# Kernel tuning notes

Measured on AMD Instinct MI355X. Metric: run time of the kernel, lower is better.

Reference implementation:

```python
import jax, jax.numpy as jnp
import numpy as np

EPS = 1e-8  # matches torch cosine_similarity default eps


def setup_inputs() -> dict:
    key = jax.random.key(0)
    k1, k2 = jax.random.split(key)
    B, S, D = 64, 512, 768
    logits = jax.random.normal(k1, (B, S, D), dtype=jnp.float32)
    labels = jax.random.randint(k2, (B, S), 0, 10, dtype=jnp.int64)
    return {"logits": logits, "labels": labels, "entity_id": 5}


def reference(logits, labels, entity_id):
    # --- get_proto: mean of token vectors whose label == entity_id,
    # excluding sequence position 0 (label_idx.remove(0) in the original) ---
    B, S, D = logits.shape
    pos = jnp.arange(S)
    ent_mask = (labels == entity_id) & (pos[None, :] != 0)      # [B,S]
    m = ent_mask.astype(logits.dtype)
    num_ent = jnp.maximum(m.sum(), 1.0)
    proto = jnp.einsum('bs,bsd->d', m, logits) / num_ent        # [D]

    # --- CLLoss: mean cosine similarity between proto and every token
    # with a nonzero label ---
    nz_mask = (labels != 0).astype(logits.dtype)                # [B,S]
    dots = jnp.einsum('bsd,d->bs', logits, proto)               # [B,S]
    denom = jnp.linalg.norm(logits, axis=-1) * jnp.linalg.norm(proto)
    sims = dots / jnp.maximum(denom, EPS)                       # [B,S]
    num_tok = jnp.maximum(nz_mask.sum(), 1.0)
    loss = (sims * nz_mask).sum() / num_tok
    return loss
```

## Files before the change

kernel.cpp:

```cpp
#include <hip/hip_runtime.h>
#include <math.h>

#define DD 768
#define S_LEN 512
#define NF4 3

__global__ __launch_bounds__(256) void zero_acc(float* acc, int n) {
    int i = blockIdx.x * 256 + threadIdx.x;
    if (i < n) acc[i] = 0.f;
}

__global__ __launch_bounds__(256) void main_pass(const float* __restrict__ logits,
                                                 const int* __restrict__ labels,
                                                 const int* __restrict__ eid_p,
                                                 int ntok,
                                                 float* __restrict__ acc) {
    const int eid  = *eid_p;
    const int lane = threadIdx.x & 63;
    const int wid  = threadIdx.x >> 6;
    const int gw   = blockIdx.x * 4 + wid;
    const int nw   = gridDim.x * 4;

    float u_acc[12], p_acc[12];
#pragma unroll
    for (int j = 0; j < 12; ++j) { u_acc[j] = 0.f; p_acc[j] = 0.f; }
    float tokcnt = 0.f;

    for (int t = gw; t < ntok; t += nw) {
        const float4* src = (const float4*)(logits + (size_t)t * DD);
        float4 f[NF4];
#pragma unroll
        for (int k = 0; k < NF4; ++k) f[k] = src[k * 64 + lane];

        float ss = 0.f;
#pragma unroll
        for (int k = 0; k < NF4; ++k)
            ss += f[k].x * f[k].x + f[k].y * f[k].y + f[k].z * f[k].z + f[k].w * f[k].w;
#pragma unroll
        for (int o = 32; o > 0; o >>= 1) ss += __shfl_xor(ss, o, 64);

        const int lbl = labels[t];
        const float inv = (ss > 0.f) ? rsqrtf(ss) : 0.f;
        const float wu  = (lbl != 0) ? inv : 0.f;
        const float wp  = (lbl == eid && (t & (S_LEN - 1)) != 0) ? 1.f : 0.f;
        tokcnt += (lbl != 0) ? 1.f : 0.f;

#pragma unroll
        for (int k = 0; k < NF4; ++k) {
            u_acc[4 * k + 0] += f[k].x * wu;  p_acc[4 * k + 0] += f[k].x * wp;
            u_acc[4 * k + 1] += f[k].y * wu;  p_acc[4 * k + 1] += f[k].y * wp;
            u_acc[4 * k + 2] += f[k].z * wu;  p_acc[4 * k + 2] += f[k].z * wp;
            u_acc[4 * k + 3] += f[k].w * wu;  p_acc[4 * k + 3] += f[k].w * wp;
        }
    }

    __shared__ float sh[2 * DD + 1];
    for (int i = threadIdx.x; i < 2 * DD + 1; i += 256) sh[i] = 0.f;
    __syncthreads();
    for (int w = 0; w < 4; ++w) {
        if (wid == w) {
#pragma unroll
            for (int k = 0; k < NF4; ++k) {
                const int d = k * 256 + lane * 4;
                sh[d + 0]      += u_acc[4 * k + 0];
                sh[d + 1]      += u_acc[4 * k + 1];
                sh[d + 2]      += u_acc[4 * k + 2];
                sh[d + 3]      += u_acc[4 * k + 3];
                sh[DD + d + 0] += p_acc[4 * k + 0];
                sh[DD + d + 1] += p_acc[4 * k + 1];
                sh[DD + d + 2] += p_acc[4 * k + 2];
                sh[DD + d + 3] += p_acc[4 * k + 3];
            }
            if (lane == 0) sh[2 * DD] += tokcnt;
        }
        __syncthreads();
    }

    for (int i = threadIdx.x; i < 2 * DD + 1; i += 256) atomicAdd(&acc[i], sh[i]);
}

__global__ __launch_bounds__(256) void finalize(const float* __restrict__ acc,
                                                float* __restrict__ out) {
    const int tid = threadIdx.x;
    double dup = 0.0, dpp = 0.0;
    for (int i = tid; i < DD; i += 256) {
        const double u = (double)acc[i];
        const double p = (double)acc[DD + i];
        dup += u * p;
        dpp += p * p;
    }
#pragma unroll
    for (int o = 32; o > 0; o >>= 1) {
        dup += __shfl_down(dup, o, 64);
        dpp += __shfl_down(dpp, o, 64);
    }
    __shared__ double s_up[4], s_pp[4];
    const int lane = tid & 63, wid = tid >> 6;
    if (lane == 0) { s_up[wid] = dup; s_pp[wid] = dpp; }
    __syncthreads();
    if (tid == 0) {
        double up = 0.0, pp = 0.0;
        for (int w = 0; w < 4; ++w) { up += s_up[w]; pp += s_pp[w]; }
        const float cnt = acc[2 * DD];
        float res = 0.f;
        if (pp > 0.0) res = (float)(up / (sqrt(pp) * (double)fmaxf(cnt, 1.f)));
        out[0] = res;
    }
}

extern "C" void kernel_launch(void* const* d_in, const int* in_sizes, int n_in,
                              void* d_out, int out_size, void* d_ws, size_t ws_size,
                              hipStream_t stream) {
    const float* logits = (const float*)d_in[0];
    const int*   labels = (const int*)d_in[1];
    const int*   eid    = (const int*)d_in[2];
    const int ntok = in_sizes[1];
    float* acc = (float*)d_ws;

    zero_acc<<<7, 256, 0, stream>>>(acc, 2 * DD + 1);
    main_pass<<<1024, 256, 0, stream>>>(logits, labels, eid, ntok, acc);
    finalize<<<1, 256, 0, stream>>>(acc, (float*)d_out);
}
```

Measured before the change: 166.5 us.

## Replace global atomics with per-block partials and two-token unrolled main loop

Each block now writes its 1537 accumulated values to its own row of a partial buffer instead of doing atomicAdd into one shared accumulator. A new reduce kernel sums the rows in chunks of 64 blocks and issues far fewer atomics. The main loop also processes two tokens per iteration so more loads are in flight. The cost is an extra kernel launch and a few MB of partial-buffer traffic, plus higher register pressure from the doubled loads.

```diff
diff --git a/kernel.cpp b/kernel.cpp
--- a/kernel.cpp
+++ b/kernel.cpp
@@ -4,6 +4,10 @@
 #define DD 768
 #define S_LEN 512
 #define NF4 3
+#define NACC (2 * DD + 1)
+#define PW 1544
+#define GMAIN 1024
+#define BCHUNK 64
 
 __global__ __launch_bounds__(256) void zero_acc(float* acc, int n) {
     int i = blockIdx.x * 256 + threadIdx.x;
@@ -14,48 +18,68 @@
                                                  const int* __restrict__ labels,
                                                  const int* __restrict__ eid_p,
                                                  int ntok,
-                                                 float* __restrict__ acc) {
+                                                 float* __restrict__ partial) {
     const int eid  = *eid_p;
     const int lane = threadIdx.x & 63;
     const int wid  = threadIdx.x >> 6;
     const int gw   = blockIdx.x * 4 + wid;
-    const int nw   = gridDim.x * 4;
+    const int nw   = GMAIN * 4;
 
     float u_acc[12], p_acc[12];
 #pragma unroll
     for (int j = 0; j < 12; ++j) { u_acc[j] = 0.f; p_acc[j] = 0.f; }
     float tokcnt = 0.f;
 
-    for (int t = gw; t < ntok; t += nw) {
-        const float4* src = (const float4*)(logits + (size_t)t * DD);
-        float4 f[NF4];
+    for (int t = gw; t < ntok; t += 2 * nw) {
+        const int t2 = t + nw;
+        const bool has2 = (t2 < ntok);
+
+        const float4* src0 = (const float4*)(logits + (size_t)t * DD);
+        const float4* src1 = (const float4*)(logits + (size_t)(has2 ? t2 : t) * DD);
+        float4 f0[NF4], f1[NF4];
 #pragma unroll
-        for (int k = 0; k < NF4; ++k) f[k] = src[k * 64 + lane];
+        for (int k = 0; k < NF4; ++k) f0[k] = src0[k * 64 + lane];
+#pragma unroll
+        for (int k = 0; k < NF4; ++k) f1[k] = src1[k * 64 + lane];
 
-        float ss = 0.f;
+        float ss0 = 0.f, ss1 = 0.f;
 #pragma unroll
-        for (int k = 0; k < NF4; ++k)
-            ss += f[k].x * f[k].x + f[k].y * f[k].y + f[k].z * f[k].z + f[k].w * f[k].w;
+        for (int k = 0; k < NF4; ++k) {
+            ss0 += f0[k].x * f0[k].x + f0[k].y * f0[k].y + f0[k].z * f0[k].z + f0[k].w * f0[k].w;
+            ss1 += f1[k].x * f1[k].x + f1[k].y * f1[k].y + f1[k].z * f1[k].z + f1[k].w * f1[k].w;
+        }
 #pragma unroll
-        for (int o = 32; o > 0; o >>= 1) ss += __shfl_xor(ss, o, 64);
+        for (int o = 32; o > 0; o >>= 1) {
+            ss0 += __shfl_xor(ss0, o, 64);
+            ss1 += __shfl_xor(ss1, o, 64);
+        }
 
-        const int lbl = labels[t];
-        const float inv = (ss > 0.f) ? rsqrtf(ss) : 0.f;
-        const float wu  = (lbl != 0) ? inv : 0.f;
-        const float wp  = (lbl == eid && (t & (S_LEN - 1)) != 0) ? 1.f : 0.f;
-        tokcnt += (lbl != 0) ? 1.f : 0.f;
+        const int lbl0 = labels[t];
+        const int lbl1 = has2 ? labels[t2] : 0;
+
+        const float inv0 = (ss0 > 0.f) ? rsqrtf(ss0) : 0.f;
+        const float inv1 = (ss1 > 0.f) ? rsqrtf(ss1) : 0.f;
+        const float wu0  = (lbl0 != 0) ? inv0 : 0.f;
+        const float wu1  = (has2 && lbl1 != 0) ? inv1 : 0.f;
+        const float wp0  = (lbl0 == eid && (t & (S_LEN - 1)) != 0) ? 1.f : 0.f;
+        const float wp1  = (has2 && lbl1 == eid && (t2 & (S_LEN - 1)) != 0) ? 1.f : 0.f;
+        tokcnt += ((lbl0 != 0) ? 1.f : 0.f) + ((has2 && lbl1 != 0) ? 1.f : 0.f);
 
 #pragma unroll
         for (int k = 0; k < NF4; ++k) {
-            u_acc[4 * k + 0] += f[k].x * wu;  p_acc[4 * k + 0] += f[k].x * wp;
-            u_acc[4 * k + 1] += f[k].y * wu;  p_acc[4 * k + 1] += f[k].y * wp;
-            u_acc[4 * k + 2] += f[k].z * wu;  p_acc[4 * k + 2] += f[k].z * wp;
-            u_acc[4 * k + 3] += f[k].w * wu;  p_acc[4 * k + 3] += f[k].w * wp;
+            u_acc[4 * k + 0] += f0[k].x * wu0 + f1[k].x * wu1;
+            u_acc[4 * k + 1] += f0[k].y * wu0 + f1[k].y * wu1;
+            u_acc[4 * k + 2] += f0[k].z * wu0 + f1[k].z * wu1;
+            u_acc[4 * k + 3] += f0[k].w * wu0 + f1[k].w * wu1;
+            p_acc[4 * k + 0] += f0[k].x * wp0 + f1[k].x * wp1;
+            p_acc[4 * k + 1] += f0[k].y * wp0 + f1[k].y * wp1;
+            p_acc[4 * k + 2] += f0[k].z * wp0 + f1[k].z * wp1;
+            p_acc[4 * k + 3] += f0[k].w * wp0 + f1[k].w * wp1;
         }
     }
 
-    __shared__ float sh[2 * DD + 1];
-    for (int i = threadIdx.x; i < 2 * DD + 1; i += 256) sh[i] = 0.f;
+    __shared__ float sh[NACC];
+    for (int i = threadIdx.x; i < NACC; i += 256) sh[i] = 0.f;
     __syncthreads();
     for (int w = 0; w < 4; ++w) {
         if (wid == w) {
@@ -76,7 +100,24 @@
         __syncthreads();
     }
 
-    for (int i = threadIdx.x; i < 2 * DD + 1; i += 256) atomicAdd(&acc[i], sh[i]);
+    float* row = partial + (size_t)blockIdx.x * PW;
+    for (int i = threadIdx.x; i < NACC; i += 256) row[i] = sh[i];
+}
+
+__global__ __launch_bounds__(256) void reduce_partials(const float* __restrict__ partial,
+                                                       float* __restrict__ acc) {
+    const int i = blockIdx.x * 256 + threadIdx.x;
+    if (i >= NACC) return;
+    const int b0 = blockIdx.y * BCHUNK;
+    float s0 = 0.f, s1 = 0.f, s2 = 0.f, s3 = 0.f;
+#pragma unroll 4
+    for (int j = 0; j < BCHUNK; j += 4) {
+        s0 += partial[(size_t)(b0 + j + 0) * PW + i];
+        s1 += partial[(size_t)(b0 + j + 1) * PW + i];
+        s2 += partial[(size_t)(b0 + j + 2) * PW + i];
+        s3 += partial[(size_t)(b0 + j + 3) * PW + i];
+    }
+    atomicAdd(&acc[i], (s0 + s1) + (s2 + s3));
 }
 
 __global__ __launch_bounds__(256) void finalize(const float* __restrict__ acc,
@@ -115,9 +156,12 @@
     const int*   labels = (const int*)d_in[1];
     const int*   eid    = (const int*)d_in[2];
     const int ntok = in_sizes[1];
-    float* acc = (float*)d_ws;
 
-    zero_acc<<<7, 256, 0, stream>>>(acc, 2 * DD + 1);
-    main_pass<<<1024, 256, 0, stream>>>(logits, labels, eid, ntok, acc);
+    float* acc     = (float*)d_ws;
+    float* partial = (float*)d_ws + 2048;
+
+    zero_acc<<<7, 256, 0, stream>>>(acc, NACC);
+    main_pass<<<GMAIN, 256, 0, stream>>>(logits, labels, eid, ntok, partial);
+    reduce_partials<<<dim3(7, GMAIN / BCHUNK), 256, 0, stream>>>(partial, acc);
     finalize<<<1, 256, 0, stream>>>(acc, (float*)d_out);
 }
```

Result: faster. 162.2 us (-2.6%).
